# Kernel optimization log

Measured on AMD Instinct MI355X. Metric: run time of the kernel, lower is better.

The kernel has to match this reference:

```python
import jax, jax.numpy as jnp
import numpy as np


def setup_inputs() -> dict:
    key = jax.random.key(0)
    k1, k2, k3, k4 = jax.random.split(key, 4)
    N, M, D, C = 8192, 8192, 512, 128
    ref_feats = jax.random.normal(k1, (N, D), dtype=jnp.float32)
    src_feats = jax.random.normal(k2, (M, D), dtype=jnp.float32)
    # pairwise_distance(..., normalized=True) assumes unit-norm features
    ref_feats = ref_feats / jnp.linalg.norm(ref_feats, axis=-1, keepdims=True)
    src_feats = src_feats / jnp.linalg.norm(src_feats, axis=-1, keepdims=True)
    cas_score0 = jax.random.uniform(k3, (C, N), dtype=jnp.float32)
    cas_score1 = jax.random.uniform(k4, (C, M), dtype=jnp.float32)
    return {
        "ref_feats": ref_feats,
        "src_feats": src_feats,
        "cas_score0": cas_score0,
        "cas_score1": cas_score1,
        "num_correspondences": 256,
    }


def reference(ref_feats, src_feats, cas_score0, cas_score1, num_correspondences):
    # masks are None -> all superpoints kept, ref_indices/src_indices = arange
    N = ref_feats.shape[0]
    M = src_feats.shape[0]
    # pairwise_distance(normalized=True): d = 2 - 2 * <ref, src>
    inner = jnp.einsum('nd,md->nm', ref_feats, src_feats)
    matching_scores = jnp.exp(-(2.0 - 2.0 * inner))  # [N, M]
    # dual normalization (row-wise and col-wise)
    ref_ms = matching_scores / jnp.sum(matching_scores, axis=1, keepdims=True)
    src_ms = matching_scores / jnp.sum(matching_scores, axis=0, keepdims=True)
    matching_scores = ref_ms * src_ms
    # overlap matrix: [N, M]
    overlap = jnp.einsum('cn,cm->nm', cas_score0, cas_score1)
    matching_scores = matching_scores * overlap
    k = min(num_correspondences, N * M)
    corr_scores, corr_indices = jax.lax.top_k(matching_scores.reshape(-1), k)
    ref_corr_indices = corr_indices // M
    src_corr_indices = corr_indices % M
    return ref_corr_indices, src_corr_indices, corr_scores
```

## Files before the change

kernel.cpp:

```cpp
#include <hip/hip_runtime.h>
#include <algorithm>
#include <cstdint>

#define Nn 8192
#define Mm 8192
#define Dd 512
#define Cc 128

#define BT  128
#define TK  16

#define KERNEL_OCC __launch_bounds__(256, 2)

#define WS_SR    0ull
#define WS_SC    65536ull
#define WS_CTR   131072ull
#define WS_GHC   131136ull
#define WS_GHF   132160ull
#define WS_FINAL 133184ull
#define WS_CAND  165952ull
#define WS_INNER 25331776ull
#define RSTORE   7296
#define WS_NEED  (WS_INNER + (size_t)RSTORE * Mm * 4ull)
#define FCAP     4096u

__device__ __forceinline__ int jcol(int tx, int j) {
  return (j < 4) ? tx * 4 + j : 64 + tx * 4 + (j - 4);
}

__device__ __forceinline__ void inner_gemm(const float* __restrict__ A,
                                           const float* __restrict__ B,
                                           int n0, int m0, int tid,
                                           float (*SA)[TK][BT], float (*SB)[TK][BT],
                                           float acc2[8][8]) {
  const int tx = tid & 15, ty = tid >> 4;
  const int lrow = tid >> 1;
  const int lk8  = (tid & 1) * 8;
  const float* Ap = A + (size_t)(n0 + lrow) * Dd + lk8;
  const float* Bp = B + (size_t)(m0 + lrow) * Dd + lk8;

#pragma unroll
  for (int i = 0; i < 8; ++i)
#pragma unroll
    for (int j = 0; j < 8; ++j) acc2[i][j] = 0.0f;

  float4 pa0 = *(const float4*)(Ap);
  float4 pa1 = *(const float4*)(Ap + 4);
  float4 pb0 = *(const float4*)(Bp);
  float4 pb1 = *(const float4*)(Bp + 4);

  int p = 0;
  for (int k0 = 0; k0 < Dd; k0 += TK) {
    {
      const float ar[8] = {pa0.x,pa0.y,pa0.z,pa0.w,pa1.x,pa1.y,pa1.z,pa1.w};
      const float br[8] = {pb0.x,pb0.y,pb0.z,pb0.w,pb1.x,pb1.y,pb1.z,pb1.w};
#pragma unroll
      for (int s = 0; s < 8; ++s) { SA[p][lk8 + s][lrow] = ar[s]; SB[p][lk8 + s][lrow] = br[s]; }
    }
    if (k0 + TK < Dd) {
      pa0 = *(const float4*)(Ap + k0 + TK);
      pa1 = *(const float4*)(Ap + k0 + TK + 4);
      pb0 = *(const float4*)(Bp + k0 + TK);
      pb1 = *(const float4*)(Bp + k0 + TK + 4);
    }
    __syncthreads();
#pragma unroll
    for (int h = 0; h < 2; ++h) {
      float t[4][8];
#pragma unroll
      for (int i = 0; i < 4; ++i)
#pragma unroll
        for (int j = 0; j < 8; ++j) t[i][j] = 0.0f;
#pragma unroll
      for (int kk = 0; kk < TK; ++kk) {
        const float4 av  = *(const float4*)&SA[p][kk][ty * 8 + h * 4];
        const float4 bv0 = *(const float4*)&SB[p][kk][tx * 4];
        const float4 bv1 = *(const float4*)&SB[p][kk][64 + tx * 4];
        const float a[4] = {av.x, av.y, av.z, av.w};
        const float b[8] = {bv0.x,bv0.y,bv0.z,bv0.w,bv1.x,bv1.y,bv1.z,bv1.w};
#pragma unroll
        for (int i = 0; i < 4; ++i)
#pragma unroll
          for (int j = 0; j < 8; ++j) t[i][j] = fmaf(a[i], b[j], t[i][j]);
      }
#pragma unroll
      for (int i = 0; i < 4; ++i)
#pragma unroll
        for (int j = 0; j < 8; ++j) acc2[h * 4 + i][j] += t[i][j];
    }
    p ^= 1;
  }
}

template<bool STORE>
__global__ KERNEL_OCC void k_pass1(const float* __restrict__ A,
                                   const float* __restrict__ B,
                                   double* __restrict__ Sr,
                                   double* __restrict__ Sc,
                                   float* __restrict__ inner) {
  __shared__ float SA[2][TK][BT];
  __shared__ float SB[2][TK][BT];
  __shared__ double csum[BT];
  const int tid = threadIdx.x;
  const int tx = tid & 15, ty = tid >> 4;
  const int n0 = blockIdx.y * BT, m0 = blockIdx.x * BT;

  float acc2[8][8];
  inner_gemm(A, B, n0, m0, tid, SA, SB, acc2);

  if (STORE && n0 < RSTORE) {
#pragma unroll
    for (int i = 0; i < 8; ++i) {
      float* rowp = inner + (size_t)(n0 + ty * 8 + i) * Mm + m0;
      *(float4*)(rowp + tx * 4)      = make_float4(acc2[i][0], acc2[i][1], acc2[i][2], acc2[i][3]);
      *(float4*)(rowp + 64 + tx * 4) = make_float4(acc2[i][4], acc2[i][5], acc2[i][6], acc2[i][7]);
    }
  }

  if (tid < BT) csum[tid] = 0.0;
  __syncthreads();

  float cp[8];
#pragma unroll
  for (int j = 0; j < 8; ++j) cp[j] = 0.0f;

#pragma unroll
  for (int i = 0; i < 8; ++i) {
    float r = 0.0f;
#pragma unroll
    for (int j = 0; j < 8; ++j) {
      const float e = expf(2.0f * acc2[i][j] - 2.0f);
      r += e;
      cp[j] += e;
    }
    double v = (double)r;
    v += __shfl_xor(v, 1, 16);
    v += __shfl_xor(v, 2, 16);
    v += __shfl_xor(v, 4, 16);
    v += __shfl_xor(v, 8, 16);
    if (tx == 0) atomicAdd(&Sr[n0 + ty * 8 + i], v);
  }
#pragma unroll
  for (int j = 0; j < 8; ++j) {
    double v = (double)cp[j];
    v += __shfl_xor(v, 16, 64);
    v += __shfl_xor(v, 32, 64);
    if ((tid & 63) < 16) atomicAdd(&csum[jcol(tx, j)], v);
  }
  __syncthreads();
  if (tid < BT) atomicAdd(&Sc[m0 + tid], csum[tid]);
}

__global__ void k_recip(double* __restrict__ Sr, double* __restrict__ Sc) {
  const int i = blockIdx.x * 256 + threadIdx.x;
  if (i < Nn) Sr[i] = 1.0 / Sr[i];
  if (i < Mm) Sc[i] = 1.0 / Sc[i];
}

template<typename FE>
__device__ __forceinline__ void select_push(const unsigned (*sb)[4], FE&& fe,
                                            int n0, int m0, int hh, int tid,
                                            unsigned int* h1, unsigned int* h2,
                                            unsigned int* wsum, unsigned int* sh_misc,
                                            uint2* __restrict__ cand,
                                            unsigned int* __restrict__ ctr,
                                            unsigned int cap) {
  const int tx = tid & 15, ty = tid >> 4;

  h1[tid] = 0; h2[tid] = 0;
  __syncthreads();
#pragma unroll
  for (int i = 0; i < 8; ++i)
#pragma unroll
    for (int j = 0; j < 4; ++j) atomicAdd(&h1[sb[i][j] >> 24], 1u);
  __syncthreads();
  if (tid < 64) {
    const int b0 = tid * 4;
    const unsigned s4 = h1[b0] + h1[b0 + 1] + h1[b0 + 2] + h1[b0 + 3];
    unsigned suf = s4;
#pragma unroll
    for (int d = 1; d < 64; d <<= 1) {
      const unsigned v = __shfl_down(suf, d, 64);
      if (tid + d < 64) suf += v;
    }
    const unsigned long long mk = __ballot(suf >= 256u);
    const int L = 63 - __builtin_clzll(mk);
    if (tid == L) {
      unsigned cum = suf - s4;
      unsigned cb = (unsigned)(4 * L), abv = cum;
      for (int b = 4 * L + 3; b >= 4 * L; --b) {
        const unsigned nc = cum + h1[b];
        if (nc >= 256u) { cb = (unsigned)b; abv = cum; break; }
        cum = nc;
      }
      sh_misc[0] = cb; sh_misc[1] = abv;
    }
  }
  __syncthreads();
  const unsigned cb = sh_misc[0], above = sh_misc[1];
#pragma unroll
  for (int i = 0; i < 8; ++i)
#pragma unroll
    for (int j = 0; j < 4; ++j)
      if ((sb[i][j] >> 24) == cb) atomicAdd(&h2[(sb[i][j] >> 16) & 0xFFu], 1u);
  __syncthreads();
  if (tid < 64) {
    const int b0 = tid * 4;
    const unsigned s4 = h2[b0] + h2[b0 + 1] + h2[b0 + 2] + h2[b0 + 3];
    unsigned suf = s4;
#pragma unroll
    for (int d = 1; d < 64; d <<= 1) {
      const unsigned v = __shfl_down(suf, d, 64);
      if (tid + d < 64) suf += v;
    }
    const unsigned long long mk = __ballot(above + suf >= 256u);
    const int L = 63 - __builtin_clzll(mk);
    if (tid == L) {
      unsigned cum = above + suf - s4;
      unsigned tb = cb << 8;
      for (int b = 4 * L + 3; b >= 4 * L; --b) {
        cum += h2[b];
        if (cum >= 256u) { tb = (cb << 8) | (unsigned)b; break; }
      }
      const unsigned old = atomicMax(&ctr[2], tb);
      sh_misc[2] = tb > old ? tb : old;
    }
  }
  __syncthreads();
  const unsigned tb16 = sh_misc[2];
  const unsigned F = tb16 > 2u ? tb16 - 2u : 0u;

  unsigned cnt = 0;
#pragma unroll
  for (int i = 0; i < 8; ++i)
#pragma unroll
    for (int j = 0; j < 4; ++j) cnt += ((sb[i][j] >> 16) >= F) ? 1u : 0u;
  const int lane = tid & 63, wv = tid >> 6;
  unsigned incl = cnt;
#pragma unroll
  for (int d = 1; d < 64; d <<= 1) {
    const unsigned nv = __shfl_up(incl, d, 64);
    if (lane >= d) incl += nv;
  }
  if (lane == 63) wsum[wv] = incl;
  __syncthreads();
  if (tid == 0) {
    unsigned run = 0;
#pragma unroll
    for (int w = 0; w < 4; ++w) { const unsigned c = wsum[w]; wsum[w] = run; run += c; }
    sh_misc[3] = atomicAdd(&ctr[0], run);
  }
  __syncthreads();
  unsigned pos = sh_misc[3] + wsum[wv] + incl - cnt;
#pragma unroll
  for (int i = 0; i < 8; ++i)
#pragma unroll
    for (int j = 0; j < 4; ++j) {
      if ((sb[i][j] >> 16) >= F) {
        if (pos < cap) {
          const unsigned idxv = ((unsigned)(n0 + ty * 8 + i) << 13)
                              | (unsigned)(m0 + hh * 64 + tx * 4 + j);
          cand[pos] = make_uint2(fe(i, j), idxv);
        }
        ++pos;
      }
    }
  __syncthreads();
}

template<bool RELOAD>
__global__ KERNEL_OCC void k_pass2(
    const float* __restrict__ A, const float* __restrict__ B,
    const float* __restrict__ C0, const float* __restrict__ C1,
    const double* __restrict__ invSr, const double* __restrict__ invSc,
    const float* __restrict__ inner, int yoff,
    uint2* __restrict__ cand, unsigned int* __restrict__ ctr, unsigned int cap) {
  __shared__ float SA[2][TK][BT];
  __shared__ float SB[2][TK][BT];
  __shared__ unsigned int h1[256];
  __shared__ unsigned int h2[256];
  __shared__ unsigned int wsum[4];
  __shared__ unsigned int sh_misc[4];
  __shared__ double dsr[BT];
  __shared__ double dsc[BT];
  __shared__ float dsrf[BT];
  __shared__ float dscf[BT];
  const int tid = threadIdx.x;
  const int tx = tid & 15, ty = tid >> 4;
  const int n0 = (blockIdx.y + yoff) * BT, m0 = blockIdx.x * BT;

  if (tid < BT) {
    const double v = invSr[n0 + tid];
    dsr[tid] = v; dsrf[tid] = (float)v;
  } else {
    const double v = invSc[m0 + tid - BT];
    dsc[tid - BT] = v; dscf[tid - BT] = (float)v;
  }

  const int frow = tid >> 4;
  const int fn   = (tid & 15) * 8;

  if (RELOAD) {
#pragma unroll 1
    for (int hh = 0; hh < 2; ++hh) {
      float ov[8][4];
#pragma unroll
      for (int i = 0; i < 8; ++i)
#pragma unroll
        for (int j = 0; j < 4; ++j) ov[i][j] = 0.0f;

      const float* c0p = C0 + (size_t)frow * Nn + n0 + fn;
      const float* c1p = C1 + (size_t)frow * Mm + m0 + fn;
      float4 ca0 = *(const float4*)(c0p);
      float4 ca1 = *(const float4*)(c0p + 4);
      float4 cb0 = *(const float4*)(c1p);
      float4 cb1 = *(const float4*)(c1p + 4);
      int p = 0;
      for (int c0i = 0; c0i < Cc; c0i += TK) {
        *(float4*)&SA[p][frow][fn]     = ca0;
        *(float4*)&SA[p][frow][fn + 4] = ca1;
        *(float4*)&SB[p][frow][fn]     = cb0;
        *(float4*)&SB[p][frow][fn + 4] = cb1;
        if (c0i + TK < Cc) {
          const size_t off = (size_t)(c0i + TK);
          ca0 = *(const float4*)(c0p + off * Nn);
          ca1 = *(const float4*)(c0p + off * Nn + 4);
          cb0 = *(const float4*)(c1p + off * Mm);
          cb1 = *(const float4*)(c1p + off * Mm + 4);
        }
        __syncthreads();
#pragma unroll
        for (int g = 0; g < 2; ++g) {
          float th[4][4];
#pragma unroll
          for (int i = 0; i < 4; ++i)
#pragma unroll
            for (int j = 0; j < 4; ++j) th[i][j] = 0.0f;
#pragma unroll
          for (int kk = 0; kk < TK; ++kk) {
            const float4 av = *(const float4*)&SA[p][kk][ty * 8 + g * 4];
            const float4 bv = *(const float4*)&SB[p][kk][hh * 64 + tx * 4];
            const float a[4] = {av.x, av.y, av.z, av.w};
            const float b[4] = {bv.x, bv.y, bv.z, bv.w};
#pragma unroll
            for (int i = 0; i < 4; ++i)
#pragma unroll
              for (int j = 0; j < 4; ++j) th[i][j] = fmaf(a[i], b[j], th[i][j]);
          }
#pragma unroll
          for (int i = 0; i < 4; ++i)
#pragma unroll
            for (int j = 0; j < 4; ++j) ov[g * 4 + i][j] += th[i][j];
        }
        p ^= 1;
      }

      float af[8][4];
      unsigned sb[8][4];
#pragma unroll
      for (int i = 0; i < 8; ++i) {
        *(float4*)&af[i][0] = *(const float4*)(inner + (size_t)(n0 + ty * 8 + i) * Mm
                                               + m0 + hh * 64 + tx * 4);
#pragma unroll
        for (int j = 0; j < 4; ++j) {
          const float ef = __expf(2.0f * af[i][j] - 2.0f);
          const float sf = ef * ef * dsrf[ty * 8 + i] * dscf[hh * 64 + tx * 4 + j]
                         * ov[i][j];
          sb[i][j] = __float_as_uint(sf);
        }
      }
      auto fe = [&](int i, int j) -> unsigned {
        const double e = exp(2.0 * (double)af[i][j] - 2.0);
        const double s = e * e * dsr[ty * 8 + i] * dsc[hh * 64 + tx * 4 + j]
                       * (double)ov[i][j];
        return __float_as_uint((float)s);
      };
      select_push(sb, fe, n0, m0, hh, tid, h1, h2, wsum, sh_misc, cand, ctr, cap);
    }
  } else {
    float acc2[8][8];
    inner_gemm(A, B, n0, m0, tid, SA, SB, acc2);

#pragma unroll 1
    for (int hh = 0; hh < 2; ++hh) {
      float ov[8][4];
#pragma unroll
      for (int i = 0; i < 8; ++i)
#pragma unroll
        for (int j = 0; j < 4; ++j) ov[i][j] = 0.0f;
      for (int c0i = 0; c0i < Cc; c0i += TK) {
        __syncthreads();
        *(float4*)&SA[0][frow][fn]     = *(const float4*)(C0 + (size_t)(c0i + frow) * Nn + n0 + fn);
        *(float4*)&SA[0][frow][fn + 4] = *(const float4*)(C0 + (size_t)(c0i + frow) * Nn + n0 + fn + 4);
        *(float4*)&SB[0][frow][fn]     = *(const float4*)(C1 + (size_t)(c0i + frow) * Mm + m0 + fn);
        *(float4*)&SB[0][frow][fn + 4] = *(const float4*)(C1 + (size_t)(c0i + frow) * Mm + m0 + fn + 4);
        __syncthreads();
#pragma unroll
        for (int g = 0; g < 2; ++g) {
          float th[4][4];
#pragma unroll
          for (int i = 0; i < 4; ++i)
#pragma unroll
            for (int j = 0; j < 4; ++j) th[i][j] = 0.0f;
#pragma unroll
          for (int kk = 0; kk < TK; ++kk) {
            const float4 av = *(const float4*)&SA[0][kk][ty * 8 + g * 4];
            const float4 bv = *(const float4*)&SB[0][kk][hh * 64 + tx * 4];
            const float a[4] = {av.x, av.y, av.z, av.w};
            const float b[4] = {bv.x, bv.y, bv.z, bv.w};
#pragma unroll
            for (int i = 0; i < 4; ++i)
#pragma unroll
              for (int j = 0; j < 4; ++j) th[i][j] = fmaf(a[i], b[j], th[i][j]);
          }
#pragma unroll
          for (int i = 0; i < 4; ++i)
#pragma unroll
            for (int j = 0; j < 4; ++j) ov[g * 4 + i][j] += th[i][j];
        }
      }

      unsigned sb[8][4];
#pragma unroll
      for (int i = 0; i < 8; ++i)
#pragma unroll
        for (int j = 0; j < 4; ++j) {
          const double e = exp(2.0 * (double)acc2[i][hh * 4 + j] - 2.0);
          const double s = e * e * dsr[ty * 8 + i] * dsc[hh * 64 + tx * 4 + j]
                         * (double)ov[i][j];
          sb[i][j] = __float_as_uint(s);
        }
      auto fe = [&](int i, int j) -> unsigned { return sb[i][j]; };
      select_push(sb, fe, n0, m0, hh, tid, h1, h2, wsum, sh_misc, cand, ctr, cap);
    }
  }
}

__global__ __launch_bounds__(256) void k_histc(const uint2* __restrict__ cand,
                                               const unsigned int* __restrict__ ctr,
                                               unsigned int cap,
                                               unsigned int* __restrict__ ghc) {
  __shared__ unsigned int lh[256];
  const int tid = threadIdx.x;
  lh[tid] = 0;
  __syncthreads();
  const unsigned n = min(ctr[0], cap);
  const unsigned stride = gridDim.x * blockDim.x;
  for (unsigned i = blockIdx.x * blockDim.x + tid; i < n; i += stride)
    atomicAdd(&lh[cand[i].x >> 24], 1u);
  __syncthreads();
  if (lh[tid]) atomicAdd(&ghc[tid], lh[tid]);
}

__global__ __launch_bounds__(256) void k_threshc(const unsigned int* __restrict__ ghc,
                                                 unsigned int* __restrict__ ctr) {
  __shared__ unsigned int g[256];
  const int tid = threadIdx.x;
  g[tid] = ghc[tid];
  __syncthreads();
  if (tid == 0) {
    unsigned cum = 0;
    for (int b = 255; b >= 0; --b) {
      cum += g[b];
      if (cum >= 256u) { ctr[4] = (unsigned)b; ctr[5] = cum - g[b]; break; }
    }
  }
}

__global__ __launch_bounds__(256) void k_histf(const uint2* __restrict__ cand,
                                               const unsigned int* __restrict__ ctr,
                                               unsigned int cap,
                                               unsigned int* __restrict__ ghf) {
  __shared__ unsigned int lh[256];
  const int tid = threadIdx.x;
  lh[tid] = 0;
  __syncthreads();
  const unsigned n = min(ctr[0], cap);
  const unsigned cb = ctr[4];
  const unsigned stride = gridDim.x * blockDim.x;
  for (unsigned i = blockIdx.x * blockDim.x + tid; i < n; i += stride) {
    const unsigned k = cand[i].x;
    if ((k >> 24) == cb) atomicAdd(&lh[(k >> 16) & 0xFFu], 1u);
  }
  __syncthreads();
  if (lh[tid]) atomicAdd(&ghf[tid], lh[tid]);
}

__global__ __launch_bounds__(256) void k_threshf(const unsigned int* __restrict__ ghf,
                                                 unsigned int* __restrict__ ctr) {
  __shared__ unsigned int g[256];
  const int tid = threadIdx.x;
  g[tid] = ghf[tid];
  __syncthreads();
  if (tid == 0) {
    const unsigned cb = ctr[4];
    unsigned cum = ctr[5], tb = cb << 8;
    for (int b = 255; b >= 0; --b) {
      cum += g[b];
      if (cum >= 256u) { tb = (cb << 8) | (unsigned)b; break; }
    }
    ctr[3] = tb;
  }
}

__global__ void k_collect(const uint2* __restrict__ cand,
                          unsigned int* __restrict__ ctr,
                          unsigned int cap, uint2* __restrict__ fin) {
  const unsigned n = min(ctr[0], cap);
  const unsigned tb = ctr[3];
  const unsigned stride = gridDim.x * blockDim.x;
  for (unsigned i = blockIdx.x * blockDim.x + threadIdx.x; i < n; i += stride) {
    const uint2 c = cand[i];
    if ((c.x >> 16) >= tb) {
      const unsigned p = atomicAdd(&ctr[1], 1u);
      if (p < FCAP) fin[p] = c;
    }
  }
}

__global__ __launch_bounds__(256) void k_sort(const uint2* __restrict__ fin,
                                              const unsigned int* __restrict__ ctr,
                                              float* __restrict__ out) {
  __shared__ unsigned long long kk[FCAP];
  const int tid = threadIdx.x;
  const unsigned n = min(ctr[1], FCAP);
  unsigned np2 = 256;
  while (np2 < n) np2 <<= 1;
  for (unsigned i = tid; i < np2; i += 256) {
    if (i < n) {
      const uint2 c = fin[i];
      kk[i] = ((unsigned long long)c.x << 32) | (unsigned long long)(c.y ^ 0xFFFFFFFFu);
    } else {
      kk[i] = 0ull;
    }
  }
  __syncthreads();
  for (unsigned k2 = 2; k2 <= np2; k2 <<= 1) {
    for (unsigned j = k2 >> 1; j > 0; j >>= 1) {
      for (unsigned i = tid; i < np2; i += 256) {
        const unsigned l = i ^ j;
        if (l > i) {
          const unsigned long long ka = kk[i], kb = kk[l];
          const bool aBefore = ka > kb;
          const bool dsc = (i & k2) == 0;
          const bool sw = dsc ? !aBefore : aBefore;
          if (sw) { kk[i] = kb; kk[l] = ka; }
        }
      }
      __syncthreads();
    }
  }
  {
    const unsigned long long kv = kk[tid];
    const unsigned key = (unsigned)(kv >> 32);
    const unsigned ix  = ((unsigned)kv) ^ 0xFFFFFFFFu;
    out[tid]        = (float)(ix >> 13);
    out[256 + tid]  = (float)(ix & 8191u);
    out[512 + tid]  = __uint_as_float(key);
  }
}

extern "C" void kernel_launch(void* const* d_in, const int* in_sizes, int n_in,
                              void* d_out, int out_size, void* d_ws, size_t ws_size,
                              hipStream_t stream) {
  (void)in_sizes; (void)n_in; (void)out_size;
  const float* ref = (const float*)d_in[0];
  const float* src = (const float*)d_in[1];
  const float* c0  = (const float*)d_in[2];
  const float* c1  = (const float*)d_in[3];
  char* ws = (char*)d_ws;
  double* Sr = (double*)(ws + WS_SR);
  double* Sc = (double*)(ws + WS_SC);
  unsigned int* ctr = (unsigned int*)(ws + WS_CTR);
  unsigned int* ghc = (unsigned int*)(ws + WS_GHC);
  unsigned int* ghf = (unsigned int*)(ws + WS_GHF);
  uint2* fin   = (uint2*)(ws + WS_FINAL);
  uint2* cand  = (uint2*)(ws + WS_CAND);
  float* inner = (float*)(ws + WS_INNER);

  const bool store = ws_size >= (size_t)WS_NEED;
  unsigned int cap;
  if (store) {
    cap = (unsigned int)((WS_INNER - WS_CAND) / 8);
  } else {
    cap = (ws_size > WS_CAND + 8)
        ? (unsigned int)std::min<size_t>((ws_size - WS_CAND) / 8, (size_t)(16u << 20))
        : 0u;
  }

  hipMemsetAsync(d_ws, 0, (size_t)WS_FINAL, stream);

  dim3 g1(Mm / BT, Nn / BT);
  if (store) {
    k_pass1<true><<<g1, 256, 0, stream>>>(ref, src, Sr, Sc, inner);
    k_recip<<<32, 256, 0, stream>>>(Sr, Sc);
    dim3 gre(Mm / BT, RSTORE / BT);
    dim3 grc(Mm / BT, (Nn - RSTORE) / BT);
    k_pass2<true><<<gre, 256, 0, stream>>>(ref, src, c0, c1, Sr, Sc, inner, 0, cand, ctr, cap);
    k_pass2<false><<<grc, 256, 0, stream>>>(ref, src, c0, c1, Sr, Sc, nullptr, RSTORE / BT, cand, ctr, cap);
  } else {
    k_pass1<false><<<g1, 256, 0, stream>>>(ref, src, Sr, Sc, nullptr);
    k_recip<<<32, 256, 0, stream>>>(Sr, Sc);
    k_pass2<false><<<g1, 256, 0, stream>>>(ref, src, c0, c1, Sr, Sc, nullptr, 0, cand, ctr, cap);
  }
  k_histc<<<256, 256, 0, stream>>>(cand, ctr, cap, ghc);
  k_threshc<<<1, 256, 0, stream>>>(ghc, ctr);
  k_histf<<<256, 256, 0, stream>>>(cand, ctr, cap, ghf);
  k_threshf<<<1, 256, 0, stream>>>(ghf, ctr);
  k_collect<<<256, 256, 0, stream>>>(cand, ctr, cap, fin);
  k_sort<<<1, 256, 0, stream>>>(fin, ctr, (float*)d_out);
}
```

Baseline: 1.722 ms.

## Merge pass2 launches with recompute rows first and skip per-tile histograms

The two k_pass2 launches, one reloading the stored inner products and one recomputing the GEMM, become a single launch. Block-row ordering puts the compute-heavy recompute rows first so they overlap with the cheaper reload tiles and there is one fewer launch tail. In select_push, each tile first reads the current global threshold and counts how many of its values reach it. If fewer than 256 do, the tile skips both histogram passes and the atomicMax and pushes its candidates using the global threshold. This saves shared-memory atomics and syncs per tile, at the cost of an extra global atomic read and a reduction.

Result: slower. 1.822 ms (+5.9%).

```diff
diff --git a/kernel.cpp b/kernel.cpp
--- a/kernel.cpp
+++ b/kernel.cpp
@@ -21,6 +21,7 @@
 #define WS_CAND  165952ull
 #define WS_INNER 25331776ull
 #define RSTORE   7296
+#define RCROWS   7
 #define WS_NEED  (WS_INNER + (size_t)RSTORE * Mm * 4ull)
 #define FCAP     4096u
 
@@ -166,76 +167,99 @@
                                             unsigned int* __restrict__ ctr,
                                             unsigned int cap) {
   const int tx = tid & 15, ty = tid >> 4;
+  const int lane = tid & 63, wv = tid >> 6;
 
   h1[tid] = 0; h2[tid] = 0;
-  __syncthreads();
+  if (tid == 0) sh_misc[0] = atomicMax(&ctr[2], 0u);
+  __syncthreads();
+  const unsigned rb = sh_misc[0];
+
+  {
+    unsigned cdec = 0;
+#pragma unroll
+    for (int i = 0; i < 8; ++i)
+#pragma unroll
+      for (int j = 0; j < 4; ++j) cdec += ((sb[i][j] >> 16) >= rb) ? 1u : 0u;
+#pragma unroll
+    for (int d = 1; d < 64; d <<= 1) cdec += __shfl_down(cdec, d, 64);
+    if (lane == 0) wsum[wv] = cdec;
+  }
+  __syncthreads();
+  if (tid == 0) sh_misc[1] = wsum[0] + wsum[1] + wsum[2] + wsum[3];
+  __syncthreads();
+  const bool skip = sh_misc[1] < 256u;
+
+  unsigned tb16;
+  if (!skip) {
+#pragma unroll
+    for (int i = 0; i < 8; ++i)
+#pragma unroll
+      for (int j = 0; j < 4; ++j) atomicAdd(&h1[sb[i][j] >> 24], 1u);
+    __syncthreads();
+    if (tid < 64) {
+      const int b0 = tid * 4;
+      const unsigned s4 = h1[b0] + h1[b0 + 1] + h1[b0 + 2] + h1[b0 + 3];
+      unsigned suf = s4;
+#pragma unroll
+      for (int d = 1; d < 64; d <<= 1) {
+        const unsigned v = __shfl_down(suf, d, 64);
+        if (tid + d < 64) suf += v;
+      }
+      const unsigned long long mk = __ballot(suf >= 256u);
+      const int L = 63 - __builtin_clzll(mk);
+      if (tid == L) {
+        unsigned cum = suf - s4;
+        unsigned cb = (unsigned)(4 * L), abv = cum;
+        for (int b = 4 * L + 3; b >= 4 * L; --b) {
+          const unsigned nc = cum + h1[b];
+          if (nc >= 256u) { cb = (unsigned)b; abv = cum; break; }
+          cum = nc;
+        }
+        sh_misc[0] = cb; sh_misc[1] = abv;
+      }
+    }
+    __syncthreads();
+    const unsigned cb = sh_misc[0], above = sh_misc[1];
+#pragma unroll
+    for (int i = 0; i < 8; ++i)
+#pragma unroll
+      for (int j = 0; j < 4; ++j)
+        if ((sb[i][j] >> 24) == cb) atomicAdd(&h2[(sb[i][j] >> 16) & 0xFFu], 1u);
+    __syncthreads();
+    if (tid < 64) {
+      const int b0 = tid * 4;
+      const unsigned s4 = h2[b0] + h2[b0 + 1] + h2[b0 + 2] + h2[b0 + 3];
+      unsigned suf = s4;
+#pragma unroll
+      for (int d = 1; d < 64; d <<= 1) {
+        const unsigned v = __shfl_down(suf, d, 64);
+        if (tid + d < 64) suf += v;
+      }
+      const unsigned long long mk = __ballot(above + suf >= 256u);
+      const int L = 63 - __builtin_clzll(mk);
+      if (tid == L) {
+        unsigned cum = above + suf - s4;
+        unsigned tb = cb << 8;
+        for (int b = 4 * L + 3; b >= 4 * L; --b) {
+          cum += h2[b];
+          if (cum >= 256u) { tb = (cb << 8) | (unsigned)b; break; }
+        }
+        const unsigned old = atomicMax(&ctr[2], tb);
+        sh_misc[2] = tb > old ? tb : old;
+      }
+    }
+    __syncthreads();
+    tb16 = sh_misc[2];
+  } else {
+    tb16 = rb;
+  }
+  const unsigned F = tb16 > 2u ? tb16 - 2u : 0u;
+
+  unsigned cnt = 0;
 #pragma unroll
   for (int i = 0; i < 8; ++i)
 #pragma unroll
-    for (int j = 0; j < 4; ++j) atomicAdd(&h1[sb[i][j] >> 24], 1u);
-  __syncthreads();
-  if (tid < 64) {
-    const int b0 = tid * 4;
-    const unsigned s4 = h1[b0] + h1[b0 + 1] + h1[b0 + 2] + h1[b0 + 3];
-    unsigned suf = s4;
-#pragma unroll
-    for (int d = 1; d < 64; d <<= 1) {
-      const unsigned v = __shfl_down(suf, d, 64);
-      if (tid + d < 64) suf += v;
-    }
-    const unsigned long long mk = __ballot(suf >= 256u);
-    const int L = 63 - __builtin_clzll(mk);
-    if (tid == L) {
-      unsigned cum = suf - s4;
-      unsigned cb = (unsigned)(4 * L), abv = cum;
-      for (int b = 4 * L + 3; b >= 4 * L; --b) {
-        const unsigned nc = cum + h1[b];
-        if (nc >= 256u) { cb = (unsigned)b; abv = cum; break; }
-        cum = nc;
-      }
-      sh_misc[0] = cb; sh_misc[1] = abv;
-    }
-  }
-  __syncthreads();
-  const unsigned cb = sh_misc[0], above = sh_misc[1];
-#pragma unroll
-  for (int i = 0; i < 8; ++i)
-#pragma unroll
-    for (int j = 0; j < 4; ++j)
-      if ((sb[i][j] >> 24) == cb) atomicAdd(&h2[(sb[i][j] >> 16) & 0xFFu], 1u);
-  __syncthreads();
-  if (tid < 64) {
-    const int b0 = tid * 4;
-    const unsigned s4 = h2[b0] + h2[b0 + 1] + h2[b0 + 2] + h2[b0 + 3];
-    unsigned suf = s4;
-#pragma unroll
-    for (int d = 1; d < 64; d <<= 1) {
-      const unsigned v = __shfl_down(suf, d, 64);
-      if (tid + d < 64) suf += v;
-    }
-    const unsigned long long mk = __ballot(above + suf >= 256u);
-    const int L = 63 - __builtin_clzll(mk);
-    if (tid == L) {
-      unsigned cum = above + suf - s4;
-      unsigned tb = cb << 8;
-      for (int b = 4 * L + 3; b >= 4 * L; --b) {
-        cum += h2[b];
-        if (cum >= 256u) { tb = (cb << 8) | (unsigned)b; break; }
-      }
-      const unsigned old = atomicMax(&ctr[2], tb);
-      sh_misc[2] = tb > old ? tb : old;
-    }
-  }
-  __syncthreads();
-  const unsigned tb16 = sh_misc[2];
-  const unsigned F = tb16 > 2u ? tb16 - 2u : 0u;
-
-  unsigned cnt = 0;
-#pragma unroll
-  for (int i = 0; i < 8; ++i)
-#pragma unroll
     for (int j = 0; j < 4; ++j) cnt += ((sb[i][j] >> 16) >= F) ? 1u : 0u;
-  const int lane = tid & 63, wv = tid >> 6;
   unsigned incl = cnt;
 #pragma unroll
   for (int d = 1; d < 64; d <<= 1) {
@@ -268,12 +292,11 @@
   __syncthreads();
 }
 
-template<bool RELOAD>
 __global__ KERNEL_OCC void k_pass2(
     const float* __restrict__ A, const float* __restrict__ B,
     const float* __restrict__ C0, const float* __restrict__ C1,
     const double* __restrict__ invSr, const double* __restrict__ invSc,
-    const float* __restrict__ inner, int yoff,
+    const float* __restrict__ inner, int mode,
     uint2* __restrict__ cand, unsigned int* __restrict__ ctr, unsigned int cap) {
   __shared__ float SA[2][TK][BT];
   __shared__ float SB[2][TK][BT];
@@ -287,7 +310,17 @@
   __shared__ float dscf[BT];
   const int tid = threadIdx.x;
   const int tx = tid & 15, ty = tid >> 4;
-  const int n0 = (blockIdx.y + yoff) * BT, m0 = blockIdx.x * BT;
+
+  bool reload;
+  int nrow;
+  if (mode == 0) {
+    reload = (blockIdx.y >= RCROWS);
+    nrow = reload ? (int)blockIdx.y - RCROWS : RSTORE / BT + (int)blockIdx.y;
+  } else {
+    reload = false;
+    nrow = (int)blockIdx.y;
+  }
+  const int n0 = nrow * BT, m0 = blockIdx.x * BT;
 
   if (tid < BT) {
     const double v = invSr[n0 + tid];
@@ -300,7 +333,7 @@
   const int frow = tid >> 4;
   const int fn   = (tid & 15) * 8;
 
-  if (RELOAD) {
+  if (reload) {
 #pragma unroll 1
     for (int hh = 0; hh < 2; ++hh) {
       float ov[8][4];
@@ -594,14 +627,12 @@
   if (store) {
     k_pass1<true><<<g1, 256, 0, stream>>>(ref, src, Sr, Sc, inner);
     k_recip<<<32, 256, 0, stream>>>(Sr, Sc);
-    dim3 gre(Mm / BT, RSTORE / BT);
-    dim3 grc(Mm / BT, (Nn - RSTORE) / BT);
-    k_pass2<true><<<gre, 256, 0, stream>>>(ref, src, c0, c1, Sr, Sc, inner, 0, cand, ctr, cap);
-    k_pass2<false><<<grc, 256, 0, stream>>>(ref, src, c0, c1, Sr, Sc, nullptr, RSTORE / BT, cand, ctr, cap);
+    k_pass2<<<dim3(Mm / BT, Nn / BT), 256, 0, stream>>>(
+        ref, src, c0, c1, Sr, Sc, inner, 0, cand, ctr, cap);
   } else {
     k_pass1<false><<<g1, 256, 0, stream>>>(ref, src, Sr, Sc, nullptr);
     k_recip<<<32, 256, 0, stream>>>(Sr, Sc);
-    k_pass2<false><<<g1, 256, 0, stream>>>(ref, src, c0, c1, Sr, Sc, nullptr, 0, cand, ctr, cap);
+    k_pass2<<<g1, 256, 0, stream>>>(ref, src, c0, c1, Sr, Sc, nullptr, 1, cand, ctr, cap);
   }
   k_histc<<<256, 256, 0, stream>>>(cand, ctr, cap, ghc);
   k_threshc<<<1, 256, 0, stream>>>(ghc, ctr);
```
